# Optimization experiments

Hardware: AMD Instinct MI355X
Metric: run time of the kernel (lower is better)

The kernel has to match this reference:

```python
import jax, jax.numpy as jnp
import numpy as np

T = 128          # timesteps
N_NODES = 32
E = 512          # edges per timestep
IN_C = 64
HID = 128
SEQ_LEN = 16
OUT_C = (4, 2)
Y_DIM = 4


def setup_inputs() -> dict:
    key = jax.random.key(0)
    ks = jax.random.split(key, 16)
    s = 0.05
    f = jnp.float32
    inp = {
        'x': jax.random.normal(ks[0], (T, N_NODES, IN_C), f),
        'edge_index': jax.random.randint(ks[1], (T, 2, E), 0, N_NODES),
        'masks': jnp.ones((T, N_NODES), dtype=bool),
        'y': jax.random.normal(ks[2], (T, N_NODES, Y_DIM), f),
        'W1': jax.random.normal(ks[3], (IN_C, HID), f) * s,
        'b1': jnp.zeros((HID,), f),
        'W2': jax.random.normal(ks[4], (HID, HID), f) * s,
        'b2': jnp.zeros((HID,), f),
        # per-node LSTM layer 1 (torch gate order i,f,g,o)
        'Wih1': jax.random.normal(ks[5], (N_NODES, 4 * HID, HID), f) * s,
        'Whh1': jax.random.normal(ks[6], (N_NODES, 4 * HID, HID), f) * s,
        'bih1': jnp.zeros((N_NODES, 4 * HID), f),
        'bhh1': jnp.zeros((N_NODES, 4 * HID), f),
        # per-node LSTM layer 2
        'Wih2': jax.random.normal(ks[7], (N_NODES, 4 * HID, HID), f) * s,
        'Whh2': jax.random.normal(ks[8], (N_NODES, 4 * HID, HID), f) * s,
        'bih2': jnp.zeros((N_NODES, 4 * HID), f),
        'bhh2': jnp.zeros((N_NODES, 4 * HID), f),
        # per-node fc hidden->hidden
        'Wfc': jax.random.normal(ks[9], (N_NODES, HID, HID), f) * s,
        'bfc': jnp.zeros((N_NODES, HID), f),
        # per-node output heads
        'Wout0': jax.random.normal(ks[10], (N_NODES, OUT_C[0], HID), f) * s,
        'bout0': jnp.zeros((N_NODES, OUT_C[0]), f),
        'Wout1': jax.random.normal(ks[11], (N_NODES, OUT_C[1], HID), f) * s,
        'bout1': jnp.zeros((N_NODES, OUT_C[1]), f),
    }
    return inp


def _gcn(x_t, ei_t, W, b):
    # PyG GCNConv: add self-loops, symmetric normalization, out[col] += norm * (xW)[row]
    n = x_t.shape[0]
    loop = jnp.arange(n)
    row = jnp.concatenate([ei_t[0], loop])
    col = jnp.concatenate([ei_t[1], loop])
    deg = jax.ops.segment_sum(jnp.ones_like(col, dtype=x_t.dtype), col, num_segments=n)
    dinv = jnp.where(deg > 0, deg ** -0.5, 0.0)
    norm = dinv[row] * dinv[col]
    h = x_t @ W
    return jax.ops.segment_sum(norm[:, None] * h[row], col, num_segments=n) + b


def _lstm(seq, Wih, Whh, bih, bhh):
    # seq: [B, L, H]; torch LSTM, gates (i,f,g,o)
    xg = jnp.einsum('blh,gh->blg', seq, Wih) + bih + bhh    # [B,L,4H]
    xg = jnp.swapaxes(xg, 0, 1)                              # [L,B,4H]
    B, H = seq.shape[0], Whh.shape[1]
    def step(carry, g_x):
        h, c = carry
        g = g_x + h @ Whh.T
        i, fgt, gg, o = jnp.split(g, 4, axis=-1)
        c = jax.nn.sigmoid(fgt) * c + jax.nn.sigmoid(i) * jnp.tanh(gg)
        h = jax.nn.sigmoid(o) * jnp.tanh(c)
        return (h, c), h
    h0 = jnp.zeros((B, H), seq.dtype)
    _, hs = jax.lax.scan(step, (h0, h0), xg)
    return jnp.swapaxes(hs, 0, 1)                            # [B,L,H]


def reference(x, edge_index, masks, y, W1, b1, W2, b2,
              Wih1, Whh1, bih1, bhh1, Wih2, Whh2, bih2, bhh2,
              Wfc, bfc, Wout0, bout0, Wout1, bout1):
    # per-timestep 2-layer GCN with relu (dropout is identity in eval mode)
    def gcn_pair(xt, et):
        h = jax.nn.relu(_gcn(xt, et, W1, b1))
        return jax.nn.relu(_gcn(h, et, W2, b2))
    h = jax.vmap(gcn_pair)(x, edge_index)                    # [T,N,H]

    # generate_sequences_node: sliding windows of length SEQ_LEN over masked
    # event features, zero-padded at the front. masks are all-ones here so
    # events == timesteps and max_events == T (static shapes for jit).
    idx = jnp.arange(T)[:, None] - (SEQ_LEN - 1) + jnp.arange(SEQ_LEN)[None, :]  # [T,L]
    valid = (idx >= 0).astype(h.dtype)
    seqs = h[jnp.clip(idx, 0)] * valid[:, :, None, None]     # [T,L,N,H]
    seqs = jnp.transpose(seqs, (2, 0, 1, 3))                 # [N,T,L,H]

    o = jax.vmap(_lstm)(seqs, Wih1, Whh1, bih1, bhh1)        # per-node weights
    o = jax.vmap(_lstm)(o, Wih2, Whh2, bih2, bhh2)
    last = jax.nn.relu(o)[:, :, -1, :]                        # [N,T,H] (fc then [:, -1] == [:, -1] then fc)
    fc = jnp.einsum('nbh,nkh->nbk', last, Wfc) + bfc[:, None, :]
    o0 = jnp.einsum('nbh,nkh->nbk', fc, Wout0) + bout0[:, None, :]
    o1 = jnp.einsum('nbh,nkh->nbk', fc, Wout1) + bout1[:, None, :]
    out0 = jnp.transpose(o0, (1, 0, 2))                       # [max_events,N,out_c0]
    out1 = jnp.transpose(o1, (1, 0, 2))                       # [max_events,N,out_c1]
    # filtered targets: y[:, i, :][mask_i] padded to max_events; identity for all-ones mask
    targets = y
    return (out0, out1, targets)
```

## Files before the change

kernel.cpp:

```cpp
#include <hip/hip_runtime.h>


#define T_STEPS 128
#define HID     128
#define G4      512
#define SEQ     16

typedef unsigned short u16;
typedef unsigned int   u32;
typedef __attribute__((ext_vector_type(8))) short bf16x8;
typedef __attribute__((ext_vector_type(4))) float f32x4;
typedef __attribute__((ext_vector_type(2))) u32   u32x2;
typedef __attribute__((ext_vector_type(4))) u32   u32x4;

__device__ __forceinline__ float bf2f(u16 u) {
  union { u32 i; float f; } v; v.i = ((u32)u) << 16; return v.f;
}
__device__ __forceinline__ u16 f2bf(float f) {
  union { u32 i; float f; } v; v.f = f;
  const u32 i = v.i;
  return (u16)((i + 0x7fffu + ((i >> 16) & 1u)) >> 16);
}
__device__ __forceinline__ float sigm(float x) { return 1.f / (1.f + __expf(-x)); }
__device__ __forceinline__ float tanh_fast(float x) { return 1.f - 2.f / (1.f + __expf(2.f * x)); }
__device__ __forceinline__ float clampg(float x) { return fminf(fmaxf(x, -25.f), 25.f); }

__device__ __forceinline__ float ldf(const void* p, size_t i, int isbf) {
  return isbf ? bf2f(((const u16*)p)[i]) : ((const float*)p)[i];
}
__device__ __forceinline__ bf16x8 ld8(const void* p, size_t o, int isbf) {
  if (isbf) return *(const bf16x8*)((const u16*)p + o);
  const float* f = (const float*)p + o;
  bf16x8 r;
  #pragma unroll
  for (int j = 0; j < 8; ++j) r[j] = (short)f2bf(f[j]);
  return r;
}
__device__ __forceinline__ int lde(const int* ei, int idx, int i64) {
  return i64 ? ei[idx * 2] : ei[idx];
}

__global__ __launch_bounds__(512) void gcn_kernel(
    const void* __restrict__ x, const int* __restrict__ ei,
    const void* __restrict__ W1, const void* __restrict__ b1,
    const void* __restrict__ W2, const void* __restrict__ b2,
    u32* __restrict__ flags, u16* __restrict__ Hb)
{
  const int t = blockIdx.x;
  const int tid = threadIdx.x;
  const int wave = tid >> 6, lane = tid & 63;
  const int quad = lane >> 4, l16 = lane & 15;

  __shared__ u16 sXA[32 * 72];
  __shared__ u16 sW1T[128 * 72];
  __shared__ u16 sW2T[128 * 136];
  __shared__ u16 sAmB[32 * 40];
  __shared__ float sAm[32 * 33];
  __shared__ u16 sT[128 * 40];
  __shared__ u16 sHA[32 * 136];
  __shared__ int sdeg[32];
  __shared__ float sdinv[32];
  __shared__ int dc1, dc2;

  if (tid == 0) { dc1 = 0; dc2 = 0; }
  __syncthreads();
  if (tid < 256) {
    const u32 w = ((const u32*)x)[tid];
    const u16 lo = (u16)(w & 0xffffu);
    const float a = fabsf(bf2f(lo));
    if (lo != 0 && a >= 9.5e-7f && a <= 8.f) atomicAdd(&dc1, 1);
    if (ei[2 * tid + 1] != 0) atomicAdd(&dc2, 1);
  }
  __syncthreads();
  const int isbf = (dc1 >= 128) ? 1 : 0;
  const int i64  = (dc2 < 8) ? 1 : 0;
  if (t == 0 && tid == 0) { flags[0] = (u32)isbf; flags[1] = (u32)i64; }

  for (int idx = tid; idx < 2048; idx += 512) {
    const int m = idx >> 6, k = idx & 63;
    sXA[m * 72 + k] = f2bf(ldf(x, (size_t)t * 2048 + idx, isbf));
  }
  for (int idx = tid; idx < 8192; idx += 512) {
    const int k = idx >> 7, nn = idx & 127;
    sW1T[nn * 72 + k] = f2bf(ldf(W1, idx, isbf));
  }
  for (int idx = tid; idx < 16384; idx += 512) {
    const int k = idx >> 7, nn = idx & 127;
    sW2T[nn * 136 + k] = f2bf(ldf(W2, idx, isbf));
  }
  for (int i = tid; i < 32 * 33; i += 512) sAm[i] = 0.f;
  if (tid < 32) sdeg[tid] = 0;
  __syncthreads();
  if (tid < 512) {
    const int cd = lde(ei, t * 1024 + 512 + tid, i64);
    if ((u32)cd < 32u) atomicAdd(&sdeg[cd], 1);
  }
  __syncthreads();
  if (tid < 32) sdinv[tid] = rsqrtf((float)(sdeg[tid] + 1));
  __syncthreads();
  if (tid < 512) {
    const int r  = lde(ei, t * 1024 + tid, i64);
    const int cd = lde(ei, t * 1024 + 512 + tid, i64);
    if ((u32)r < 32u && (u32)cd < 32u)
      atomicAdd(&sAm[cd * 33 + r], sdinv[r] * sdinv[cd]);
  }
  if (tid < 32) atomicAdd(&sAm[tid * 33 + tid], sdinv[tid] * sdinv[tid]);
  __syncthreads();

  for (int idx = tid; idx < 1024; idx += 512) {
    const int m = idx >> 5, k = idx & 31;
    sAmB[m * 40 + k] = f2bf(sAm[m * 33 + k]);
  }
  {
    const int nc = wave * 16 + l16;
    f32x4 c0 = {0.f,0.f,0.f,0.f}, c1 = {0.f,0.f,0.f,0.f};
    #pragma unroll
    for (int kc = 0; kc < 2; ++kc) {
      const bf16x8 a0 = *(const bf16x8*)&sXA[l16 * 72 + kc * 32 + quad * 8];
      const bf16x8 a1 = *(const bf16x8*)&sXA[(16 + l16) * 72 + kc * 32 + quad * 8];
      const bf16x8 bb = *(const bf16x8*)&sW1T[nc * 72 + kc * 32 + quad * 8];
      c0 = __builtin_amdgcn_mfma_f32_16x16x32_bf16(a0, bb, c0, 0, 0, 0);
      c1 = __builtin_amdgcn_mfma_f32_16x16x32_bf16(a1, bb, c1, 0, 0, 0);
    }
    #pragma unroll
    for (int r = 0; r < 4; ++r) {
      sT[nc * 40 + quad * 4 + r]      = f2bf(c0[r]);
      sT[nc * 40 + 16 + quad * 4 + r] = f2bf(c1[r]);
    }
  }
  __syncthreads();
  {
    const int nc = wave * 16 + l16;
    const bf16x8 a0 = *(const bf16x8*)&sAmB[l16 * 40 + quad * 8];
    const bf16x8 a1 = *(const bf16x8*)&sAmB[(16 + l16) * 40 + quad * 8];
    const bf16x8 bb = *(const bf16x8*)&sT[nc * 40 + quad * 8];
    f32x4 c0 = {0.f,0.f,0.f,0.f}, c1 = {0.f,0.f,0.f,0.f};
    c0 = __builtin_amdgcn_mfma_f32_16x16x32_bf16(a0, bb, c0, 0, 0, 0);
    c1 = __builtin_amdgcn_mfma_f32_16x16x32_bf16(a1, bb, c1, 0, 0, 0);
    const float bv = ldf(b1, nc, isbf);
    #pragma unroll
    for (int r = 0; r < 4; ++r) {
      float v0 = c0[r] + bv, v1 = c1[r] + bv;
      sHA[(quad * 4 + r) * 136 + nc]      = f2bf(v0 > 0.f ? v0 : 0.f);
      sHA[(16 + quad * 4 + r) * 136 + nc] = f2bf(v1 > 0.f ? v1 : 0.f);
    }
  }
  __syncthreads();
  {
    const int nc = wave * 16 + l16;
    f32x4 c0 = {0.f,0.f,0.f,0.f}, c1 = {0.f,0.f,0.f,0.f};
    #pragma unroll
    for (int kc = 0; kc < 4; ++kc) {
      const bf16x8 a0 = *(const bf16x8*)&sHA[l16 * 136 + kc * 32 + quad * 8];
      const bf16x8 a1 = *(const bf16x8*)&sHA[(16 + l16) * 136 + kc * 32 + quad * 8];
      const bf16x8 bb = *(const bf16x8*)&sW2T[nc * 136 + kc * 32 + quad * 8];
      c0 = __builtin_amdgcn_mfma_f32_16x16x32_bf16(a0, bb, c0, 0, 0, 0);
      c1 = __builtin_amdgcn_mfma_f32_16x16x32_bf16(a1, bb, c1, 0, 0, 0);
    }
    #pragma unroll
    for (int r = 0; r < 4; ++r) {
      sT[nc * 40 + quad * 4 + r]      = f2bf(c0[r]);
      sT[nc * 40 + 16 + quad * 4 + r] = f2bf(c1[r]);
    }
  }
  __syncthreads();
  {
    const int nc = wave * 16 + l16;
    const bf16x8 a0 = *(const bf16x8*)&sAmB[l16 * 40 + quad * 8];
    const bf16x8 a1 = *(const bf16x8*)&sAmB[(16 + l16) * 40 + quad * 8];
    const bf16x8 bb = *(const bf16x8*)&sT[nc * 40 + quad * 8];
    f32x4 c0 = {0.f,0.f,0.f,0.f}, c1 = {0.f,0.f,0.f,0.f};
    c0 = __builtin_amdgcn_mfma_f32_16x16x32_bf16(a0, bb, c0, 0, 0, 0);
    c1 = __builtin_amdgcn_mfma_f32_16x16x32_bf16(a1, bb, c1, 0, 0, 0);
    const float bv = ldf(b2, nc, isbf);
    #pragma unroll
    for (int r = 0; r < 4; ++r) {
      float v0 = c0[r] + bv, v1 = c1[r] + bv;
      Hb[((size_t)t * 32 + quad * 4 + r) * 128 + nc]      = f2bf(v0 > 0.f ? v0 : 0.f);
      Hb[((size_t)t * 32 + 16 + quad * 4 + r) * 128 + nc] = f2bf(v1 > 0.f ? v1 : 0.f);
    }
  }
}

#define XGS 514
__global__ __launch_bounds__(512, 1) void lstm_fused_kernel(
    const void* __restrict__ Wih1, const void* __restrict__ Whh1,
    const void* __restrict__ Wih2, const void* __restrict__ Whh2,
    const void* __restrict__ bih1, const void* __restrict__ bhh1,
    const void* __restrict__ bih2, const void* __restrict__ bhh2,
    const u16* __restrict__ Hb, const u32* __restrict__ flags,
    u16* __restrict__ HLAST)
{
  const int isbf = (int)flags[0];
  const int b = blockIdx.x;
  const int n = b & 31, wg = b >> 5;
  const int t0 = wg * 16;
  const int tid = threadIdx.x;
  const int wave = tid >> 6, lane = tid & 63;
  const int quad = lane >> 4, l16 = lane & 15;

  __shared__ u16 sH1[2][16 * 136];
  __shared__ u16 sH2[2][16 * 136];
  __shared__ u16 sHB[32 * 136];
  __shared__ u16 sXG[32 * XGS];
  __shared__ float sB1[512];
  __shared__ float sB2[512];

  sB1[tid] = ldf(bih1, n * 512 + tid, isbf) + ldf(bhh1, n * 512 + tid, isbf);
  sB2[tid] = ldf(bih2, n * 512 + tid, isbf) + ldf(bhh2, n * 512 + tid, isbf);
  for (int i = tid; i < 16 * 136; i += 512) { sH1[0][i] = 0; sH2[0][i] = 0; }

  for (int idx = tid; idx < 32 * 128; idx += 512) {
    const int row = idx >> 7, cc = idx & 127;
    const int tp = t0 - 15 + row;
    sHB[row * 136 + cc] =
        (tp >= 0 && tp < T_STEPS) ? Hb[((size_t)tp * 32 + n) * 128 + cc] : (u16)0;
  }

  const size_t Wbase = (size_t)n * G4 * HID;
  bf16x8 bfr1[4][4], bfri[4][4], bfrh[4][4];
  #pragma unroll
  for (int t = 0; t < 4; ++t) {
    const int g = t * 128 + wave * 16 + l16;
    const size_t gb = Wbase + (size_t)g * HID;
    #pragma unroll
    for (int kc = 0; kc < 4; ++kc) {
      bfr1[t][kc] = ld8(Whh1, gb + kc * 32 + quad * 8, isbf);
      bfri[t][kc] = ld8(Wih2, gb + kc * 32 + quad * 8, isbf);
      bfrh[t][kc] = ld8(Whh2, gb + kc * 32 + quad * 8, isbf);
    }
  }
  __syncthreads();

  #pragma unroll
  for (int t = 0; t < 4; ++t) {
    const int g = t * 128 + wave * 16 + l16;
    const size_t gb = Wbase + (size_t)g * HID;
    f32x4 a0 = {0.f, 0.f, 0.f, 0.f}, a1 = {0.f, 0.f, 0.f, 0.f};
    #pragma unroll
    for (int kc = 0; kc < 4; ++kc) {
      const bf16x8 wf = ld8(Wih1, gb + kc * 32 + quad * 8, isbf);
      const bf16x8 h0 = *(const bf16x8*)&sHB[l16 * 136 + kc * 32 + quad * 8];
      const bf16x8 h1 = *(const bf16x8*)&sHB[(16 + l16) * 136 + kc * 32 + quad * 8];
      a0 = __builtin_amdgcn_mfma_f32_16x16x32_bf16(h0, wf, a0, 0, 0, 0);
      a1 = __builtin_amdgcn_mfma_f32_16x16x32_bf16(h1, wf, a1, 0, 0, 0);
    }
    const float bb = sB1[g];
    #pragma unroll
    for (int r = 0; r < 4; ++r) {
      sXG[(quad * 4 + r) * XGS + g]      = f2bf(a0[r] + bb);
      sXG[(16 + quad * 4 + r) * XGS + g] = f2bf(a1[r] + bb);
    }
  }

  float bias2[4];
  #pragma unroll
  for (int t = 0; t < 4; ++t) bias2[t] = sB2[t * 128 + wave * 16 + l16];

  float c1[4] = {0.f, 0.f, 0.f, 0.f};
  float c2v[4] = {0.f, 0.f, 0.f, 0.f};
  const int col = wave * 16 + l16;

  __syncthreads();

  int p = 0;
  for (int l = 0; l < SEQ; ++l) {
    {
      bf16x8 a1f[4];
      #pragma unroll
      for (int kc = 0; kc < 4; ++kc)
        a1f[kc] = *(const bf16x8*)&sH1[p][l16 * 136 + kc * 32 + quad * 8];
      f32x4 acc[4];
      #pragma unroll
      for (int t = 0; t < 4; ++t) { acc[t][0]=0.f; acc[t][1]=0.f; acc[t][2]=0.f; acc[t][3]=0.f; }
      #pragma unroll
      for (int t = 0; t < 4; ++t)
        #pragma unroll
        for (int kc = 0; kc < 4; ++kc)
          acc[t] = __builtin_amdgcn_mfma_f32_16x16x32_bf16(a1f[kc], bfr1[t][kc], acc[t], 0, 0, 0);
      #pragma unroll
      for (int r = 0; r < 4; ++r) {
        const int base = (quad * 4 + r + l) * XGS + col;
        const float gi = clampg(acc[0][r] + bf2f(sXG[base]));
        const float gf = clampg(acc[1][r] + bf2f(sXG[base + 128]));
        const float gg = clampg(acc[2][r] + bf2f(sXG[base + 256]));
        const float go = clampg(acc[3][r] + bf2f(sXG[base + 384]));
        c1[r] = sigm(gf) * c1[r] + sigm(gi) * tanh_fast(gg);
        sH1[1 - p][(quad * 4 + r) * 136 + col] = f2bf(sigm(go) * tanh_fast(c1[r]));
      }
    }
    __syncthreads();
    {
      bf16x8 ao[4], ah[4];
      #pragma unroll
      for (int kc = 0; kc < 4; ++kc) {
        ao[kc] = *(const bf16x8*)&sH1[1 - p][l16 * 136 + kc * 32 + quad * 8];
        ah[kc] = *(const bf16x8*)&sH2[p][l16 * 136 + kc * 32 + quad * 8];
      }
      f32x4 acc[4];
      #pragma unroll
      for (int t = 0; t < 4; ++t) { acc[t][0]=0.f; acc[t][1]=0.f; acc[t][2]=0.f; acc[t][3]=0.f; }
      #pragma unroll
      for (int t = 0; t < 4; ++t) {
        #pragma unroll
        for (int kc = 0; kc < 4; ++kc)
          acc[t] = __builtin_amdgcn_mfma_f32_16x16x32_bf16(ao[kc], bfri[t][kc], acc[t], 0, 0, 0);
        #pragma unroll
        for (int kc = 0; kc < 4; ++kc)
          acc[t] = __builtin_amdgcn_mfma_f32_16x16x32_bf16(ah[kc], bfrh[t][kc], acc[t], 0, 0, 0);
      }
      #pragma unroll
      for (int r = 0; r < 4; ++r) {
        const float gi = clampg(acc[0][r] + bias2[0]);
        const float gf = clampg(acc[1][r] + bias2[1]);
        const float gg = clampg(acc[2][r] + bias2[2]);
        const float go = clampg(acc[3][r] + bias2[3]);
        c2v[r] = sigm(gf) * c2v[r] + sigm(gi) * tanh_fast(gg);
        const u16 hb = f2bf(sigm(go) * tanh_fast(c2v[r]));
        sH2[1 - p][(quad * 4 + r) * 136 + col] = hb;
        if (l == SEQ - 1)
          HLAST[((size_t)n * T_STEPS + t0 + quad * 4 + r) * HID + col] = hb;
      }
    }
    __syncthreads();
    p ^= 1;
  }
}

__global__ __launch_bounds__(256) void head_kernel(
    const u16* __restrict__ HLAST, const void* __restrict__ Wfc, const void* __restrict__ bfc,
    const void* __restrict__ Wout0, const void* __restrict__ bout0,
    const void* __restrict__ Wout1, const void* __restrict__ bout1,
    const void* __restrict__ y, const u32* __restrict__ flags,
    float* __restrict__ out)
{
  const int isbf = (int)flags[0];
  const int b = blockIdx.x;
  const int n = b >> 2, tc = (b & 3) * 32;
  const int tid = threadIdx.x;
  const int wave = tid >> 6, lane = tid & 63;
  const int quad = lane >> 4, l16 = lane & 15;

  __shared__ u16 sLA[32 * 136];
  __shared__ float sF[32 * 132];

  for (int i = tid; i < 32 * 128; i += 256) {
    const int r = i >> 7, cc = i & 127;
    const u16 hv = HLAST[((size_t)n * T_STEPS + tc + r) * 128 + cc];
    const float v = bf2f(hv);
    sLA[r * 136 + cc] = v > 0.f ? hv : (u16)0;
  }
  __syncthreads();

  {
    f32x4 acc[2][2];
    #pragma unroll
    for (int mt = 0; mt < 2; ++mt)
      #pragma unroll
      for (int nt = 0; nt < 2; ++nt) { acc[mt][nt][0]=0.f; acc[mt][nt][1]=0.f; acc[mt][nt][2]=0.f; acc[mt][nt][3]=0.f; }
    #pragma unroll
    for (int kc = 0; kc < 4; ++kc) {
      const bf16x8 a0 = *(const bf16x8*)&sLA[l16 * 136 + kc * 32 + quad * 8];
      const bf16x8 a1 = *(const bf16x8*)&sLA[(16 + l16) * 136 + kc * 32 + quad * 8];
      #pragma unroll
      for (int nt = 0; nt < 2; ++nt) {
        const int col = wave * 32 + nt * 16 + l16;
        const bf16x8 bb = ld8(Wfc, (size_t)n * 16384 + (size_t)col * 128 + kc * 32 + quad * 8, isbf);
        acc[0][nt] = __builtin_amdgcn_mfma_f32_16x16x32_bf16(a0, bb, acc[0][nt], 0, 0, 0);
        acc[1][nt] = __builtin_amdgcn_mfma_f32_16x16x32_bf16(a1, bb, acc[1][nt], 0, 0, 0);
      }
    }
    #pragma unroll
    for (int nt = 0; nt < 2; ++nt) {
      const int col = wave * 32 + nt * 16 + l16;
      const float bv = ldf(bfc, n * 128 + col, isbf);
      #pragma unroll
      for (int r = 0; r < 4; ++r) {
        sF[(quad * 4 + r) * 132 + col]      = acc[0][nt][r] + bv;
        sF[(16 + quad * 4 + r) * 132 + col] = acc[1][nt][r] + bv;
      }
    }
  }
  __syncthreads();

  if (tid < 192) {
    const int tt = tid / 6, o = tid % 6;
    size_t wb; float a;
    if (o < 4) { wb = ((size_t)n * 4 + o) * 128;       a = ldf(bout0, n * 4 + o, isbf); }
    else       { wb = ((size_t)n * 2 + (o - 4)) * 128; a = ldf(bout1, n * 2 + o - 4, isbf); }
    for (int k = 0; k < 128; ++k)
      a += sF[tt * 132 + k] * (o < 4 ? ldf(Wout0, wb + k, isbf) : ldf(Wout1, wb + k, isbf));
    const int t = tc + tt;
    if (o < 4) out[((size_t)t * 32 + n) * 4 + o] = a;
    else       out[16384 + ((size_t)t * 32 + n) * 2 + (o - 4)] = a;
  }

  if (tid < 128) {
    const int tt = tid >> 2, k = tid & 3;
    const int t = tc + tt;
    const size_t i = ((size_t)t * 32 + n) * 4 + k;
    out[24576 + i] = ldf(y, i, isbf);
  }
}

extern "C" void kernel_launch(void* const* d_in, const int* in_sizes, int n_in,
                              void* d_out, int out_size, void* d_ws, size_t ws_size,
                              hipStream_t stream)
{
  (void)out_size;
  static const int DICT_M[22]  = {262144,131072,4096,16384,8192,128,16384,128,
                                  2097152,2097152,16384,16384,2097152,2097152,
                                  16384,16384,524288,4096,16384,128,8192,64};
  static const int DICT_NM[21] = {262144,131072,16384,8192,128,16384,128,
                                  2097152,2097152,16384,16384,2097152,2097152,
                                  16384,16384,524288,4096,16384,128,8192,64};
  static const int SORT_M[22]  = {8192,16384,524288,2097152,2097152,2097152,
                                  2097152,16384,8192,128,128,4096,16384,16384,
                                  16384,16384,128,64,131072,4096,262144,16384};
  static const int SORT_NM[21] = {8192,16384,524288,2097152,2097152,2097152,
                                  2097152,16384,8192,128,128,4096,16384,16384,
                                  16384,16384,128,64,131072,262144,16384};
  auto matches = [&](const int* exp, int cnt, int ei_idx) -> bool {
    if (n_in != cnt) return false;
    for (int i = 0; i < cnt; ++i) {
      if (i == ei_idx) {
        if (in_sizes[i] != 131072 && in_sizes[i] != 262144) return false;
      } else if (in_sizes[i] != exp[i]) return false;
    }
    return true;
  };
  int map[21];
  auto set_dict = [&](int sh) {
    map[0] = 0; map[1] = 1;
    for (int s = 2; s < 21; ++s) map[s] = s + 1 + sh;
  };
  auto set_sorted = [&](int xi) {
    map[0] = xi; map[1] = 18; map[2] = xi + 1;
    map[3] = 0;  map[4] = 9;  map[5] = 1;  map[6] = 10;
    map[7] = 5;  map[8] = 3;  map[9] = 14; map[10] = 12;
    map[11] = 6; map[12] = 4; map[13] = 15; map[14] = 13;
    map[15] = 2; map[16] = 11; map[17] = 7; map[18] = 16;
    map[19] = 8; map[20] = 17;
  };
  if      (matches(DICT_M, 22, 1))  set_dict(0);
  else if (matches(DICT_NM, 21, 1)) set_dict(-1);
  else if (matches(SORT_M, 22, 18)) set_sorted(20);
  else if (matches(SORT_NM, 21, 18)) set_sorted(19);
  else set_dict((n_in >= 22) ? 0 : -1);

  const void* x     = d_in[map[0]];
  const int*  ei    = (const int*)d_in[map[1]];
  const void* y     = d_in[map[2]];
  const void* W1    = d_in[map[3]];
  const void* b1    = d_in[map[4]];
  const void* W2    = d_in[map[5]];
  const void* b2    = d_in[map[6]];
  const void* Wih1  = d_in[map[7]];
  const void* Whh1  = d_in[map[8]];
  const void* bih1  = d_in[map[9]];
  const void* bhh1  = d_in[map[10]];
  const void* Wih2  = d_in[map[11]];
  const void* Whh2  = d_in[map[12]];
  const void* bih2  = d_in[map[13]];
  const void* bhh2  = d_in[map[14]];
  const void* Wfc   = d_in[map[15]];
  const void* bfc   = d_in[map[16]];
  const void* Wout0 = d_in[map[17]];
  const void* bout0 = d_in[map[18]];
  const void* Wout1 = d_in[map[19]];
  const void* bout1 = d_in[map[20]];
  float* out = (float*)d_out;

  const size_t WS_NEED = 4096 + 1048576 + 1048576;
  if (ws_size < WS_NEED) return;
  char* ws = (char*)d_ws;
  u32* flags  = (u32*)ws;
  u16* Hb     = (u16*)(ws + 4096);
  u16* HLAST  = (u16*)(ws + 4096 + 1048576);

  gcn_kernel       <<<dim3(128), dim3(512), 0, stream>>>(x, ei, W1, b1, W2, b2, flags, Hb);
  lstm_fused_kernel<<<dim3(256), dim3(512), 0, stream>>>(Wih1, Whh1, Wih2, Whh2,
                                                         bih1, bhh1, bih2, bhh2, Hb, flags, HLAST);
  head_kernel      <<<dim3(128), dim3(256), 0, stream>>>(HLAST, Wfc, bfc, Wout0, bout0, Wout1, bout1, y, flags, out);
}
```

Before: 244.2 us.

## Split fused two-layer LSTM into sequential phases to cut register pressure

```diff
diff --git a/kernel.cpp b/kernel.cpp
--- a/kernel.cpp
+++ b/kernel.cpp
@@ -10,8 +10,6 @@
 typedef unsigned int   u32;
 typedef __attribute__((ext_vector_type(8))) short bf16x8;
 typedef __attribute__((ext_vector_type(4))) float f32x4;
-typedef __attribute__((ext_vector_type(2))) u32   u32x2;
-typedef __attribute__((ext_vector_type(4))) u32   u32x4;
 
 __device__ __forceinline__ float bf2f(u16 u) {
   union { u32 i; float f; } v; v.i = ((u32)u) << 16; return v.f;
@@ -182,8 +180,9 @@
   }
 }
 
-#define XGS 514
-__global__ __launch_bounds__(512, 1) void lstm_fused_kernel(
+#define XGS   514
+#define H1STR 2176
+__global__ __launch_bounds__(512) void lstm_fused_kernel(
     const void* __restrict__ Wih1, const void* __restrict__ Whh1,
     const void* __restrict__ Wih2, const void* __restrict__ Whh2,
     const void* __restrict__ bih1, const void* __restrict__ bhh1,
@@ -198,17 +197,14 @@
   const int tid = threadIdx.x;
   const int wave = tid >> 6, lane = tid & 63;
   const int quad = lane >> 4, l16 = lane & 15;
-
-  __shared__ u16 sH1[2][16 * 136];
-  __shared__ u16 sH2[2][16 * 136];
-  __shared__ u16 sHB[32 * 136];
-  __shared__ u16 sXG[32 * XGS];
-  __shared__ float sB1[512];
-  __shared__ float sB2[512];
-
-  sB1[tid] = ldf(bih1, n * 512 + tid, isbf) + ldf(bhh1, n * 512 + tid, isbf);
-  sB2[tid] = ldf(bih2, n * 512 + tid, isbf) + ldf(bhh2, n * 512 + tid, isbf);
-  for (int i = tid; i < 16 * 136; i += 512) { sH1[0][i] = 0; sH2[0][i] = 0; }
+  const int col = wave * 16 + l16;
+
+  __shared__ __align__(16) char arena[119936];
+  u16* sHB  = (u16*)(arena);
+  u16* sXG1 = (u16*)(arena + 8704);
+  u16* xg2  = (u16*)(arena);
+  u16* h1s  = (u16*)(arena + 41600);
+  u16* sH2  = (u16*)(arena + 111232);
 
   for (int idx = tid; idx < 32 * 128; idx += 512) {
     const int row = idx >> 7, cc = idx & 127;
@@ -216,25 +212,13 @@
     sHB[row * 136 + cc] =
         (tp >= 0 && tp < T_STEPS) ? Hb[((size_t)tp * 32 + n) * 128 + cc] : (u16)0;
   }
+  __syncthreads();
 
   const size_t Wbase = (size_t)n * G4 * HID;
-  bf16x8 bfr1[4][4], bfri[4][4], bfrh[4][4];
+
   #pragma unroll
   for (int t = 0; t < 4; ++t) {
-    const int g = t * 128 + wave * 16 + l16;
-    const size_t gb = Wbase + (size_t)g * HID;
-    #pragma unroll
-    for (int kc = 0; kc < 4; ++kc) {
-      bfr1[t][kc] = ld8(Whh1, gb + kc * 32 + quad * 8, isbf);
-      bfri[t][kc] = ld8(Wih2, gb + kc * 32 + quad * 8, isbf);
-      bfrh[t][kc] = ld8(Whh2, gb + kc * 32 + quad * 8, isbf);
-    }
-  }
-  __syncthreads();
-
-  #pragma unroll
-  for (int t = 0; t < 4; ++t) {
-    const int g = t * 128 + wave * 16 + l16;
+    const int g = t * 128 + col;
     const size_t gb = Wbase + (size_t)g * HID;
     f32x4 a0 = {0.f, 0.f, 0.f, 0.f}, a1 = {0.f, 0.f, 0.f, 0.f};
     #pragma unroll
@@ -245,85 +229,126 @@
       a0 = __builtin_amdgcn_mfma_f32_16x16x32_bf16(h0, wf, a0, 0, 0, 0);
       a1 = __builtin_amdgcn_mfma_f32_16x16x32_bf16(h1, wf, a1, 0, 0, 0);
     }
-    const float bb = sB1[g];
+    const float bb = ldf(bih1, n * 512 + g, isbf) + ldf(bhh1, n * 512 + g, isbf);
     #pragma unroll
     for (int r = 0; r < 4; ++r) {
-      sXG[(quad * 4 + r) * XGS + g]      = f2bf(a0[r] + bb);
-      sXG[(16 + quad * 4 + r) * XGS + g] = f2bf(a1[r] + bb);
-    }
-  }
-
-  float bias2[4];
+      sXG1[(quad * 4 + r) * XGS + g]      = f2bf(a0[r] + bb);
+      sXG1[(16 + quad * 4 + r) * XGS + g] = f2bf(a1[r] + bb);
+    }
+  }
+
+  bf16x8 bfr1[4][4];
   #pragma unroll
-  for (int t = 0; t < 4; ++t) bias2[t] = sB2[t * 128 + wave * 16 + l16];
-
-  float c1[4] = {0.f, 0.f, 0.f, 0.f};
-  float c2v[4] = {0.f, 0.f, 0.f, 0.f};
-  const int col = wave * 16 + l16;
-
-  __syncthreads();
-
-  int p = 0;
+  for (int t = 0; t < 4; ++t) {
+    const size_t gb = Wbase + (size_t)(t * 128 + col) * HID;
+    #pragma unroll
+    for (int kc = 0; kc < 4; ++kc)
+      bfr1[t][kc] = ld8(Whh1, gb + kc * 32 + quad * 8, isbf);
+  }
+
+  float c1v[4] = {0.f, 0.f, 0.f, 0.f};
+  __syncthreads();
+
   for (int l = 0; l < SEQ; ++l) {
-    {
+    f32x4 acc[4];
+    #pragma unroll
+    for (int t = 0; t < 4; ++t) { acc[t][0]=0.f; acc[t][1]=0.f; acc[t][2]=0.f; acc[t][3]=0.f; }
+    if (l) {
       bf16x8 a1f[4];
       #pragma unroll
       for (int kc = 0; kc < 4; ++kc)
-        a1f[kc] = *(const bf16x8*)&sH1[p][l16 * 136 + kc * 32 + quad * 8];
-      f32x4 acc[4];
-      #pragma unroll
-      for (int t = 0; t < 4; ++t) { acc[t][0]=0.f; acc[t][1]=0.f; acc[t][2]=0.f; acc[t][3]=0.f; }
+        a1f[kc] = *(const bf16x8*)&h1s[(l - 1) * H1STR + l16 * 136 + kc * 32 + quad * 8];
       #pragma unroll
       for (int t = 0; t < 4; ++t)
         #pragma unroll
         for (int kc = 0; kc < 4; ++kc)
           acc[t] = __builtin_amdgcn_mfma_f32_16x16x32_bf16(a1f[kc], bfr1[t][kc], acc[t], 0, 0, 0);
-      #pragma unroll
-      for (int r = 0; r < 4; ++r) {
-        const int base = (quad * 4 + r + l) * XGS + col;
-        const float gi = clampg(acc[0][r] + bf2f(sXG[base]));
-        const float gf = clampg(acc[1][r] + bf2f(sXG[base + 128]));
-        const float gg = clampg(acc[2][r] + bf2f(sXG[base + 256]));
-        const float go = clampg(acc[3][r] + bf2f(sXG[base + 384]));
-        c1[r] = sigm(gf) * c1[r] + sigm(gi) * tanh_fast(gg);
-        sH1[1 - p][(quad * 4 + r) * 136 + col] = f2bf(sigm(go) * tanh_fast(c1[r]));
+    }
+    #pragma unroll
+    for (int r = 0; r < 4; ++r) {
+      const int base = (quad * 4 + r + l) * XGS + col;
+      const float gi = clampg(acc[0][r] + bf2f(sXG1[base]));
+      const float gf = clampg(acc[1][r] + bf2f(sXG1[base + 128]));
+      const float gg = clampg(acc[2][r] + bf2f(sXG1[base + 256]));
+      const float go = clampg(acc[3][r] + bf2f(sXG1[base + 384]));
+      c1v[r] = sigm(gf) * c1v[r] + sigm(gi) * tanh_fast(gg);
+      h1s[l * H1STR + (quad * 4 + r) * 136 + col] = f2bf(sigm(go) * tanh_fast(c1v[r]));
+    }
+    __syncthreads();
+  }
+
+  bf16x8 bfrh[4][4];
+  #pragma unroll
+  for (int t = 0; t < 4; ++t) {
+    const size_t gb = Wbase + (size_t)(t * 128 + col) * HID;
+    #pragma unroll
+    for (int kc = 0; kc < 4; ++kc)
+      bfrh[t][kc] = ld8(Whh2, gb + kc * 32 + quad * 8, isbf);
+  }
+  float bias2[4];
+  #pragma unroll
+  for (int t = 0; t < 4; ++t)
+    bias2[t] = ldf(bih2, n * 512 + t * 128 + col, isbf) +
+               ldf(bhh2, n * 512 + t * 128 + col, isbf);
+
+  float c2v[4] = {0.f, 0.f, 0.f, 0.f};
+  int p = 0;
+
+  for (int ch = 0; ch < 8; ++ch) {
+    #pragma unroll
+    for (int t = 0; t < 4; ++t) {
+      bf16x8 bfi[4];
+      const size_t gb = Wbase + (size_t)(t * 128 + col) * HID;
+      #pragma unroll
+      for (int kc = 0; kc < 4; ++kc)
+        bfi[kc] = ld8(Wih2, gb + kc * 32 + quad * 8, isbf);
+      #pragma unroll
+      for (int m = 0; m < 2; ++m) {
+        f32x4 fa = {0.f, 0.f, 0.f, 0.f};
+        #pragma unroll
+        for (int kc = 0; kc < 4; ++kc) {
+          const bf16x8 am =
+              *(const bf16x8*)&h1s[(2 * ch + m) * H1STR + l16 * 136 + kc * 32 + quad * 8];
+          fa = __builtin_amdgcn_mfma_f32_16x16x32_bf16(am, bfi[kc], fa, 0, 0, 0);
+        }
+        #pragma unroll
+        for (int r = 0; r < 4; ++r)
+          xg2[m * (16 * XGS) + (quad * 4 + r) * XGS + t * 128 + col] = f2bf(fa[r]);
       }
     }
     __syncthreads();
-    {
-      bf16x8 ao[4], ah[4];
-      #pragma unroll
-      for (int kc = 0; kc < 4; ++kc) {
-        ao[kc] = *(const bf16x8*)&sH1[1 - p][l16 * 136 + kc * 32 + quad * 8];
-        ah[kc] = *(const bf16x8*)&sH2[p][l16 * 136 + kc * 32 + quad * 8];
-      }
+    for (int m = 0; m < 2; ++m) {
+      const int s = 2 * ch + m;
       f32x4 acc[4];
       #pragma unroll
       for (int t = 0; t < 4; ++t) { acc[t][0]=0.f; acc[t][1]=0.f; acc[t][2]=0.f; acc[t][3]=0.f; }
-      #pragma unroll
-      for (int t = 0; t < 4; ++t) {
+      if (s) {
+        bf16x8 ah[4];
         #pragma unroll
         for (int kc = 0; kc < 4; ++kc)
-          acc[t] = __builtin_amdgcn_mfma_f32_16x16x32_bf16(ao[kc], bfri[t][kc], acc[t], 0, 0, 0);
+          ah[kc] = *(const bf16x8*)&sH2[p * 2176 + l16 * 136 + kc * 32 + quad * 8];
         #pragma unroll
-        for (int kc = 0; kc < 4; ++kc)
-          acc[t] = __builtin_amdgcn_mfma_f32_16x16x32_bf16(ah[kc], bfrh[t][kc], acc[t], 0, 0, 0);
+        for (int t = 0; t < 4; ++t)
+          #pragma unroll
+          for (int kc = 0; kc < 4; ++kc)
+            acc[t] = __builtin_amdgcn_mfma_f32_16x16x32_bf16(ah[kc], bfrh[t][kc], acc[t], 0, 0, 0);
       }
       #pragma unroll
       for (int r = 0; r < 4; ++r) {
-        const float gi = clampg(acc[0][r] + bias2[0]);
-        const float gf = clampg(acc[1][r] + bias2[1]);
-        const float gg = clampg(acc[2][r] + bias2[2]);
-        const float go = clampg(acc[3][r] + bias2[3]);
+        const int base = m * (16 * XGS) + (quad * 4 + r) * XGS + col;
+        const float gi = clampg(acc[0][r] + bf2f(xg2[base])       + bias2[0]);
+        const float gf = clampg(acc[1][r] + bf2f(xg2[base + 128]) + bias2[1]);
+        const float gg = clampg(acc[2][r] + bf2f(xg2[base + 256]) + bias2[2]);
+        const float go = clampg(acc[3][r] + bf2f(xg2[base + 384]) + bias2[3]);
         c2v[r] = sigm(gf) * c2v[r] + sigm(gi) * tanh_fast(gg);
         const u16 hb = f2bf(sigm(go) * tanh_fast(c2v[r]));
-        sH2[1 - p][(quad * 4 + r) * 136 + col] = hb;
-        if (l == SEQ - 1)
+        sH2[(1 - p) * 2176 + (quad * 4 + r) * 136 + col] = hb;
+        if (s == SEQ - 1)
           HLAST[((size_t)n * T_STEPS + t0 + quad * 4 + r) * HID + col] = hb;
       }
-    }
-    __syncthreads();
-    p ^= 1;
+      __syncthreads();
+      p ^= 1;
+    }
   }
 }
 
```

Result: slower. 294.0 us (+20.4%).
